# Performance work log

Measured on AMD Instinct MI355X. Metric: run time of the kernel, lower is better.

Reference implementation:

```python
import jax, jax.numpy as jnp
import numpy as np

NUM_CLASSES = 21
RMI_RADIUS = 3
POOL = 3            # rmi_pool_size == rmi_pool_stride
HALF_D = RMI_RADIUS * RMI_RADIUS
WEIGHT_LAMBDA = 0.5
CLIP_MIN = 1e-6
POS_ALPHA = 5e-4


def _max_pool(x):
    # F.max_pool2d(kernel=3, stride=3, padding=1) on NCHW
    return jax.lax.reduce_window(
        x, -jnp.inf, jax.lax.max,
        window_dimensions=(1, 1, POOL, POOL),
        window_strides=(1, 1, POOL, POOL),
        padding=[(0, 0), (0, 0), (1, 1), (1, 1)])


def _map_get_pairs(labels, probs, radius):
    # -> two tensors [N, C, radius*radius, new_h, new_w]
    h, w = labels.shape[2], labels.shape[3]
    nh, nw = h - (radius - 1), w - (radius - 1)
    la = jnp.stack([labels[:, :, y:y + nh, x:x + nw]
                    for y in range(radius) for x in range(radius)], axis=2)
    pr = jnp.stack([probs[:, :, y:y + nh, x:x + nw]
                    for y in range(radius) for x in range(radius)], axis=2)
    return la, pr


def _rmi_lower_bound(labels_4D, probs_4D):
    labels_4D = _max_pool(labels_4D)
    probs_4D = _max_pool(probs_4D)
    la, pr = _map_get_pairs(labels_4D, probs_4D, RMI_RADIUS)
    N, C = la.shape[0], la.shape[1]
    la = jax.lax.stop_gradient(la.reshape(N, C, HALF_D, -1))  # [N,C,D,M]
    pr = pr.reshape(N, C, HALF_D, -1)
    la = la - jnp.mean(la, axis=3, keepdims=True)
    pr = pr - jnp.mean(pr, axis=3, keepdims=True)
    eye = jnp.eye(HALF_D, dtype=pr.dtype) * POS_ALPHA  # broadcast over N,C
    la_cov = jnp.einsum('ncdm,ncem->ncde', la, la)
    pr_cov = jnp.einsum('ncdm,ncem->ncde', pr, pr)
    pr_cov_inv = jnp.linalg.inv(pr_cov + eye)
    la_pr_cov = jnp.einsum('ncdm,ncem->ncde', la, pr)
    appro_var = la_cov - jnp.einsum('ncde,ncef,ncgf->ncdg',
                                    la_pr_cov, pr_cov_inv, la_pr_cov)
    chol = jnp.linalg.cholesky(appro_var + eye)
    diag = jnp.diagonal(chol, axis1=-2, axis2=-1)
    rmi_now = 0.5 * 2.0 * jnp.sum(jnp.log(diag + 1e-8), axis=-1)  # [N,C]
    rmi_per_class = jnp.mean(rmi_now.reshape(-1, NUM_CLASSES), axis=0) / float(HALF_D)
    return jnp.sum(rmi_per_class)  # _IS_SUM = 1


def setup_inputs() -> dict:
    key = jax.random.key(0)
    k1, k2 = jax.random.split(key)
    logits_4D = jax.random.normal(k1, (4, NUM_CLASSES, 512, 512), dtype=jnp.float32)
    labels_4D = jax.random.randint(k2, (4, 512, 512), 0, NUM_CLASSES).astype(jnp.int64)
    return {'logits_4D': logits_4D, 'labels_4D': labels_4D}


def reference(logits_4D, labels_4D):
    # forward_sigmoid
    mask = (labels_4D < NUM_CLASSES)                       # [N,H,W] bool
    maskf = mask.astype(logits_4D.dtype)
    onehot = jax.nn.one_hot(labels_4D * mask, NUM_CLASSES,
                            dtype=logits_4D.dtype) * maskf[..., None]  # [N,H,W,C]
    onehot = jax.lax.stop_gradient(onehot)
    logits_flat = jnp.transpose(logits_4D, (0, 2, 3, 1)).reshape(-1, NUM_CLASSES)
    y_flat = onehot.reshape(-1, NUM_CLASSES)
    w_flat = maskf.reshape(-1, 1)
    valid_pixels = jnp.sum(maskf)
    # stable BCE-with-logits, sum reduction, per-pixel weight
    bce = -(y_flat * jax.nn.log_sigmoid(logits_flat)
            + (1.0 - y_flat) * jax.nn.log_sigmoid(-logits_flat))
    bce_loss = jnp.sum(bce * w_flat) / (valid_pixels + 1.0)
    probs_4D = jax.nn.sigmoid(logits_4D) * maskf[:, None, :, :] + CLIP_MIN
    labels_nchw = jnp.transpose(onehot, (0, 3, 1, 2))
    rmi_loss = _rmi_lower_bound(labels_nchw, probs_4D)
    # lambda_way == 1
    return WEIGHT_LAMBDA * bce_loss + rmi_loss * (1.0 - WEIGHT_LAMBDA)
```

## Files before the change

kernel.cpp:

```cpp
#include <hip/hip_runtime.h>
#include <math.h>
#include <stdint.h>

#define NUM_CL 21
#define NB 4
#define H 512
#define W 512
#define PH 171
#define PW 171
#define NHH 169
#define NWW 169
#define M_TOT (NHH*NWW)
#define NCP (NB*NUM_CL)
#define PPLANE (PH*PW)
#define ACC_PER 189
#define SLICES 8
#define MCHUNK ((M_TOT + SLICES - 1)/SLICES)
#define POS_ALPHA 5e-4
#define NBLKA (NB*NUM_CL*PH)

__device__ __forceinline__ int upIdx(int lo, int hi) {
    return lo*9 - (lo*(lo-1))/2 + (hi - lo);
}
__device__ __forceinline__ int tri(int d, int e) { return d*(d+1)/2 + e; }

__global__ __launch_bounds__(128) void kernelA(
    const float* __restrict__ logits, const int* __restrict__ labels,
    float* __restrict__ pooledP, unsigned char* __restrict__ pooledL,
    float* __restrict__ bce_part, unsigned int* __restrict__ cnt_part)
{
    int blk = blockIdx.x;
    int c  = blk % NUM_CL;
    int t2 = blk / NUM_CL;
    int ph = t2 % PH;
    int n  = t2 / PH;
    int q  = threadIdx.x;
    int col0 = q << 2;

    __shared__ float         svP[W];
    __shared__ unsigned char svL[W];
    __shared__ float         rbce[2];
    __shared__ unsigned int  rcnt[2];

    const float* lgp = logits + (size_t)(n*NUM_CL + c) * (H*W);
    const int*   lbp = labels + (size_t)n * (H*W);

    float vP[4] = {-INFINITY, -INFINITY, -INFINITY, -INFINITY};
    int   vL[4] = {0,0,0,0};
    float bce = 0.f;
    unsigned int cnt = 0;

    int rbase = 3*ph - 1;
    #pragma unroll
    for (int rr = 0; rr < 3; ++rr) {
        int r = rbase + rr;
        if (r < 0 || r >= H) continue;
        float4 x4 = *(const float4*)(lgp + (size_t)r*W + col0);
        int4   l4 = *(const int4*)  (lbp + (size_t)r*W + col0);
        float xs[4] = {x4.x, x4.y, x4.z, x4.w};
        int   ls[4] = {l4.x, l4.y, l4.z, l4.w};
        #pragma unroll
        for (int k = 0; k < 4; ++k) {
            int lab = ls[k];
            float x = xs[k];
            float m = (lab < NUM_CL) ? 1.f : 0.f;
            float y = (lab == c) ? 1.f : 0.f;
            float te = __expf(-fabsf(x));
            float u  = 1.f + te;
            float sp = __logf(u);
            float rc = __builtin_amdgcn_rcpf(u);
            bce += m * (fmaxf(x, 0.f) - x*y + sp);
            float sig = (x >= 0.f) ? rc : te*rc;
            float p = sig*m + 1e-6f;
            vP[k] = fmaxf(vP[k], p);
            vL[k] |= (lab == c);
            cnt += (unsigned)(lab < NUM_CL);
        }
    }

    ((float4*)svP)[q] = make_float4(vP[0], vP[1], vP[2], vP[3]);
    uchar4 u4;
    u4.x = (unsigned char)vL[0]; u4.y = (unsigned char)vL[1];
    u4.z = (unsigned char)vL[2]; u4.w = (unsigned char)vL[3];
    ((uchar4*)svL)[q] = u4;

    #pragma unroll
    for (int o = 32; o > 0; o >>= 1) {
        bce += __shfl_down(bce, o, 64);
        cnt += __shfl_down(cnt, o, 64);
    }
    int lane = threadIdx.x & 63, wv = threadIdx.x >> 6;
    if (lane == 0) { rbce[wv] = bce; rcnt[wv] = cnt; }
    __syncthreads();

    for (int pw = threadIdx.x; pw < PW; pw += 128) {
        int c0 = 3*pw - 1; if (c0 < 0) c0 = 0;
        int c1 = 3*pw + 2; if (c1 > W) c1 = W;
        float pm = -INFINITY; int lm = 0;
        for (int qq = c0; qq < c1; ++qq) {
            pm = fmaxf(pm, svP[qq]);
            lm |= svL[qq];
        }
        size_t o = ((size_t)(n*NUM_CL + c) * PH + ph) * PW + pw;
        pooledP[o] = pm;
        pooledL[o] = (unsigned char)lm;
    }

    if (threadIdx.x == 0) {
        bce_part[blk] = rbce[0] + rbce[1];
        if (c == 0) cnt_part[t2] = rcnt[0] + rcnt[1];
    }
}

__global__ __launch_bounds__(256) void kernelB(
    const float* __restrict__ pooledP, const unsigned char* __restrict__ pooledL,
    double* __restrict__ cov_acc)
{
    int nc    = blockIdx.x;
    int slice = blockIdx.y;
    int grp   = blockIdx.z;
    const float* P = pooledP + (size_t)nc * PPLANE;
    const unsigned char* L = pooledL + (size_t)nc * PPLANE;

    int mlo = slice * MCHUNK;
    int mhi = mlo + MCHUNK; if (mhi > M_TOT) mhi = M_TOT;

    __shared__ float red[4][108];
    int lane = threadIdx.x & 63;
    int wave = threadIdx.x >> 6;

    auto wred = [&](float v) -> float {
        #pragma unroll
        for (int o = 32; o > 0; o >>= 1) v += __shfl_down(v, o, 64);
        return v;
    };

    double* acc = cov_acc + (size_t)nc * ACC_PER;

    if (grp == 0) {
        float sl[9], sp[9], cll[45], cpp[45];
        #pragma unroll
        for (int d = 0; d < 9; ++d) { sl[d] = 0.f; sp[d] = 0.f; }
        #pragma unroll
        for (int k = 0; k < 45; ++k) { cll[k] = 0.f; cpp[k] = 0.f; }

        for (int m = mlo + (int)threadIdx.x; m < mhi; m += 256) {
            int i = m / NWW;
            int j = m - i * NWW;
            int base = i * PW + j;
            float la[9], pr[9];
            #pragma unroll
            for (int dy = 0; dy < 3; ++dy)
                #pragma unroll
                for (int dx = 0; dx < 3; ++dx) {
                    int o = base + dy*PW + dx;
                    pr[dy*3+dx] = P[o];
                    la[dy*3+dx] = (float)L[o];
                }
            #pragma unroll
            for (int d = 0; d < 9; ++d) { sl[d] += la[d]; sp[d] += pr[d]; }
            int k = 0;
            #pragma unroll
            for (int d = 0; d < 9; ++d)
                #pragma unroll
                for (int e = d; e < 9; ++e) {
                    cll[k] += la[d]*la[e];
                    cpp[k] += pr[d]*pr[e];
                    ++k;
                }
        }

        #pragma unroll
        for (int d = 0; d < 9; ++d) { float r = wred(sl[d]);  if (lane == 0) red[wave][d]     = r; }
        #pragma unroll
        for (int d = 0; d < 9; ++d) { float r = wred(sp[d]);  if (lane == 0) red[wave][9+d]   = r; }
        #pragma unroll
        for (int k = 0; k < 45; ++k) { float r = wred(cll[k]); if (lane == 0) red[wave][18+k] = r; }
        #pragma unroll
        for (int k = 0; k < 45; ++k) { float r = wred(cpp[k]); if (lane == 0) red[wave][63+k] = r; }
        __syncthreads();
        for (int v = threadIdx.x; v < 108; v += 256) {
            float s = red[0][v] + red[1][v] + red[2][v] + red[3][v];
            atomicAdd(&acc[v], (double)s);
        }
    } else {
        float clp[81];
        #pragma unroll
        for (int k = 0; k < 81; ++k) clp[k] = 0.f;

        for (int m = mlo + (int)threadIdx.x; m < mhi; m += 256) {
            int i = m / NWW;
            int j = m - i * NWW;
            int base = i * PW + j;
            float la[9], pr[9];
            #pragma unroll
            for (int dy = 0; dy < 3; ++dy)
                #pragma unroll
                for (int dx = 0; dx < 3; ++dx) {
                    int o = base + dy*PW + dx;
                    pr[dy*3+dx] = P[o];
                    la[dy*3+dx] = (float)L[o];
                }
            #pragma unroll
            for (int d = 0; d < 9; ++d)
                #pragma unroll
                for (int e = 0; e < 9; ++e) clp[d*9+e] += la[d]*pr[e];
        }

        #pragma unroll
        for (int k = 0; k < 81; ++k) { float r = wred(clp[k]); if (lane == 0) red[wave][k] = r; }
        __syncthreads();
        for (int v = threadIdx.x; v < 81; v += 256) {
            float s = red[0][v] + red[1][v] + red[2][v] + red[3][v];
            atomicAdd(&acc[108 + v], (double)s);
        }
    }
}

__global__ __launch_bounds__(128) void kernelC(
    const double* __restrict__ cov_acc,
    const float* __restrict__ bce_part,
    const unsigned int* __restrict__ cnt_part,
    float* __restrict__ out)
{
    int t = threadIdx.x;

    __shared__ double sb[128];
    __shared__ unsigned long long sc[128];
    double bs = 0.0;
    for (int i = t; i < NBLKA; i += 128) bs += (double)bce_part[i];
    unsigned long long cs = 0;
    for (int i = t; i < NB*PH; i += 128) cs += cnt_part[i];
    sb[t] = bs; sc[t] = cs;
    __syncthreads();
    #pragma unroll
    for (int s = 64; s > 0; s >>= 1) {
        if (t < s) { sb[t] += sb[t + s]; sc[t] += sc[t + s]; }
        __syncthreads();
    }

    float contrib = 0.f;
    if (t < NCP) {
        const double* acc = cov_acc + (size_t)t * ACC_PER;
        const double Minv = 1.0 / (double)M_TOT;
        double Sl[9], Sp[9];
        #pragma unroll
        for (int d = 0; d < 9; ++d) { Sl[d] = acc[d]; Sp[d] = acc[9+d]; }

        float A[45];
        float G[45];
        float B[81];
        #pragma unroll
        for (int d = 0; d < 9; ++d) {
            #pragma unroll
            for (int e = 0; e <= d; ++e) {
                int ku = upIdx(e, d);
                double vp = acc[63+ku] - Sp[d]*Sp[e]*Minv;
                double vl = acc[18+ku] - Sl[d]*Sl[e]*Minv;
                if (d == e) vp += POS_ALPHA;
                A[tri(d,e)] = (float)vp;
                G[tri(d,e)] = (float)vl;
            }
        }
        #pragma unroll
        for (int d = 0; d < 9; ++d) {
            #pragma unroll
            for (int e = 0; e < 9; ++e)
                B[d*9+e] = (float)(acc[108 + d*9 + e] - Sl[d]*Sp[e]*Minv);
        }

        #pragma unroll
        for (int d = 0; d < 9; ++d) {
            float s = A[tri(d,d)];
            #pragma unroll
            for (int f = 0; f < d; ++f) { float v = A[tri(d,f)]; s -= v*v; }
            float ldd = sqrtf(s);
            A[tri(d,d)] = ldd;
            float inv = 1.f / ldd;
            #pragma unroll
            for (int e = d+1; e < 9; ++e) {
                float s2 = A[tri(e,d)];
                #pragma unroll
                for (int f = 0; f < d; ++f) s2 -= A[tri(e,f)] * A[tri(d,f)];
                A[tri(e,d)] = s2 * inv;
            }
        }

        #pragma unroll
        for (int d = 0; d < 9; ++d) {
            #pragma unroll
            for (int e = 0; e < 9; ++e) {
                float s = B[d*9+e];
                #pragma unroll
                for (int f = 0; f < e; ++f) s -= A[tri(e,f)] * B[d*9+f];
                B[d*9+e] = s / A[tri(e,e)];
            }
        }

        #pragma unroll
        for (int d = 0; d < 9; ++d) {
            #pragma unroll
            for (int g = 0; g <= d; ++g) {
                float qv = 0.f;
                #pragma unroll
                for (int e = 0; e < 9; ++e) qv += B[d*9+e] * B[g*9+e];
                float v = G[tri(d,g)] - qv;
                if (d == g) v += (float)POS_ALPHA;
                G[tri(d,g)] = v;
            }
        }

        float sumlog = 0.f;
        #pragma unroll
        for (int d = 0; d < 9; ++d) {
            float s = G[tri(d,d)];
            #pragma unroll
            for (int f = 0; f < d; ++f) { float v = G[tri(d,f)]; s -= v*v; }
            float ldd = sqrtf(s);
            G[tri(d,d)] = ldd;
            sumlog += logf(ldd + 1e-8f);
            float inv = 1.f / ldd;
            #pragma unroll
            for (int e = d+1; e < 9; ++e) {
                float s2 = G[tri(e,d)];
                #pragma unroll
                for (int f = 0; f < d; ++f) s2 -= G[tri(e,f)] * G[tri(d,f)];
                G[tri(e,d)] = s2 * inv;
            }
        }
        contrib = sumlog * (1.0f / 36.0f);
    }

    __shared__ float sred[128];
    sred[t] = contrib;
    __syncthreads();
    #pragma unroll
    for (int s = 64; s > 0; s >>= 1) {
        if (t < s) sred[t] += sred[t + s];
        __syncthreads();
    }
    if (t == 0) {
        double bce_loss = sb[0] / ((double)sc[0] + 1.0);
        out[0] = (float)(0.5 * bce_loss + 0.5 * (double)sred[0]);
    }
}

extern "C" void kernel_launch(void* const* d_in, const int* in_sizes, int n_in,
                              void* d_out, int out_size, void* d_ws, size_t ws_size,
                              hipStream_t stream)
{
    (void)in_sizes; (void)n_in; (void)out_size; (void)ws_size;
    const float* logits = (const float*)d_in[0];
    const int*   labels = (const int*)d_in[1];
    float* out = (float*)d_out;

    uint8_t* w = (uint8_t*)d_ws;
    double* cov_acc = (double*)w;
    size_t off = (size_t)NCP * ACC_PER * 8;
    float* bce_part = (float*)(w + off);       off += (size_t)NBLKA * 4;
    unsigned int* cnt_part = (unsigned int*)(w + off); off += (size_t)(NB*PH) * 4;
    float* pooledP = (float*)(w + off);        off += (size_t)NCP * PPLANE * 4;
    unsigned char* pooledL = (unsigned char*)(w + off);

    hipMemsetAsync(cov_acc, 0, (size_t)NCP * ACC_PER * 8, stream);

    kernelA<<<NBLKA, 128, 0, stream>>>(logits, labels, pooledP, pooledL, bce_part, cnt_part);
    kernelB<<<dim3(NCP, SLICES, 2), 256, 0, stream>>>(pooledP, pooledL, cov_acc);
    kernelC<<<1, 128, 0, stream>>>(cov_acc, bce_part, cnt_part, out);
}
```

Baseline: 233.9 us.

## Compress labels to bytes and bitmasks, use strip-based covariance accumulation

A new pre-pass converts the int labels to a uint8 map and counts valid pixels once. Kernel A then reads 1-byte labels instead of 4-byte ones, which cuts label traffic that was re-read for each of the 21 classes. Pooled label maps are stored as 64-bit ballot bitmasks, and pooled probabilities go into rows padded to 176 for float4 loads. The covariance kernels now process 16-wide horizontal strips per thread, reusing loaded values across windows and computing the label-label statistics with popcount instead of float multiplies. The cost is an extra kernel launch and higher register pressure in the strip bodies.

```diff
diff --git a/kernel.cpp b/kernel.cpp
--- a/kernel.cpp
+++ b/kernel.cpp
@@ -8,47 +8,67 @@
 #define W 512
 #define PH 171
 #define PW 171
+#define PWPAD 176
 #define NHH 169
 #define NWW 169
 #define M_TOT (NHH*NWW)
 #define NCP (NB*NUM_CL)
-#define PPLANE (PH*PW)
 #define ACC_PER 189
-#define SLICES 8
-#define MCHUNK ((M_TOT + SLICES - 1)/SLICES)
 #define POS_ALPHA 5e-4
 #define NBLKA (NB*NUM_CL*PH)
+#define NCHUNK 11
+#define ITEMS (NHH*NCHUNK)
+#define BSLICE 8
+
+typedef unsigned long long u64;
+typedef unsigned int u32;
 
 __device__ __forceinline__ int upIdx(int lo, int hi) {
     return lo*9 - (lo*(lo-1))/2 + (hi - lo);
 }
 __device__ __forceinline__ int tri(int d, int e) { return d*(d+1)/2 + e; }
 
+__global__ __launch_bounds__(256) void kernel0(
+    const int* __restrict__ labels, unsigned char* __restrict__ lab8,
+    u64* __restrict__ validCnt)
+{
+    int idx = blockIdx.x * 256 + threadIdx.x;
+    int4 l = ((const int4*)labels)[idx];
+    uchar4 u;
+    u.x = (l.x < NUM_CL) ? (unsigned char)l.x : 255;
+    u.y = (l.y < NUM_CL) ? (unsigned char)l.y : 255;
+    u.z = (l.z < NUM_CL) ? (unsigned char)l.z : 255;
+    u.w = (l.w < NUM_CL) ? (unsigned char)l.w : 255;
+    ((uchar4*)lab8)[idx] = u;
+    u32 cnt = (l.x < NUM_CL) + (l.y < NUM_CL) + (l.z < NUM_CL) + (l.w < NUM_CL);
+    #pragma unroll
+    for (int o = 32; o > 0; o >>= 1) cnt += __shfl_down(cnt, o, 64);
+    if ((threadIdx.x & 63) == 0) atomicAdd(validCnt, (u64)cnt);
+}
+
 __global__ __launch_bounds__(128) void kernelA(
-    const float* __restrict__ logits, const int* __restrict__ labels,
-    float* __restrict__ pooledP, unsigned char* __restrict__ pooledL,
-    float* __restrict__ bce_part, unsigned int* __restrict__ cnt_part)
+    const float* __restrict__ logits, const unsigned char* __restrict__ lab8,
+    float* __restrict__ pooledP, u64* __restrict__ Lbits,
+    float* __restrict__ bce_part)
 {
     int blk = blockIdx.x;
     int c  = blk % NUM_CL;
     int t2 = blk / NUM_CL;
     int ph = t2 % PH;
     int n  = t2 / PH;
-    int q  = threadIdx.x;
-    int col0 = q << 2;
+    int tid = threadIdx.x;
+    int col0 = tid << 2;
 
     __shared__ float         svP[W];
     __shared__ unsigned char svL[W];
     __shared__ float         rbce[2];
-    __shared__ unsigned int  rcnt[2];
 
     const float* lgp = logits + (size_t)(n*NUM_CL + c) * (H*W);
-    const int*   lbp = labels + (size_t)n * (H*W);
+    const unsigned char* lbp = lab8 + (size_t)n * (H*W);
 
     float vP[4] = {-INFINITY, -INFINITY, -INFINITY, -INFINITY};
     int   vL[4] = {0,0,0,0};
     float bce = 0.f;
-    unsigned int cnt = 0;
 
     int rbase = 3*ph - 1;
     #pragma unroll
@@ -56,7 +76,7 @@
         int r = rbase + rr;
         if (r < 0 || r >= H) continue;
         float4 x4 = *(const float4*)(lgp + (size_t)r*W + col0);
-        int4   l4 = *(const int4*)  (lbp + (size_t)r*W + col0);
+        uchar4 l4 = *(const uchar4*)(lbp + (size_t)r*W + col0);
         float xs[4] = {x4.x, x4.y, x4.z, x4.w};
         int   ls[4] = {l4.x, l4.y, l4.z, l4.w};
         #pragma unroll
@@ -71,171 +91,222 @@
             float rc = __builtin_amdgcn_rcpf(u);
             bce += m * (fmaxf(x, 0.f) - x*y + sp);
             float sig = (x >= 0.f) ? rc : te*rc;
-            float p = sig*m + 1e-6f;
-            vP[k] = fmaxf(vP[k], p);
+            vP[k] = fmaxf(vP[k], sig*m + 1e-6f);
             vL[k] |= (lab == c);
-            cnt += (unsigned)(lab < NUM_CL);
-        }
-    }
-
-    ((float4*)svP)[q] = make_float4(vP[0], vP[1], vP[2], vP[3]);
+        }
+    }
+
+    ((float4*)svP)[tid] = make_float4(vP[0], vP[1], vP[2], vP[3]);
     uchar4 u4;
     u4.x = (unsigned char)vL[0]; u4.y = (unsigned char)vL[1];
     u4.z = (unsigned char)vL[2]; u4.w = (unsigned char)vL[3];
-    ((uchar4*)svL)[q] = u4;
-
-    #pragma unroll
-    for (int o = 32; o > 0; o >>= 1) {
-        bce += __shfl_down(bce, o, 64);
-        cnt += __shfl_down(cnt, o, 64);
-    }
-    int lane = threadIdx.x & 63, wv = threadIdx.x >> 6;
-    if (lane == 0) { rbce[wv] = bce; rcnt[wv] = cnt; }
+    ((uchar4*)svL)[tid] = u4;
+
+    #pragma unroll
+    for (int o = 32; o > 0; o >>= 1) bce += __shfl_down(bce, o, 64);
+    int lane = tid & 63, wv = tid >> 6;
+    if (lane == 0) rbce[wv] = bce;
     __syncthreads();
 
-    for (int pw = threadIdx.x; pw < PW; pw += 128) {
-        int c0 = 3*pw - 1; if (c0 < 0) c0 = 0;
-        int c1 = 3*pw + 2; if (c1 > W) c1 = W;
-        float pm = -INFINITY; int lm = 0;
-        for (int qq = c0; qq < c1; ++qq) {
-            pm = fmaxf(pm, svP[qq]);
-            lm |= svL[qq];
-        }
-        size_t o = ((size_t)(n*NUM_CL + c) * PH + ph) * PW + pw;
-        pooledP[o] = pm;
-        pooledL[o] = (unsigned char)lm;
-    }
-
-    if (threadIdx.x == 0) {
-        bce_part[blk] = rbce[0] + rbce[1];
-        if (c == 0) cnt_part[t2] = rcnt[0] + rcnt[1];
-    }
-}
-
-__global__ __launch_bounds__(256) void kernelB(
-    const float* __restrict__ pooledP, const unsigned char* __restrict__ pooledL,
+    size_t rowr = (size_t)(n*NUM_CL + c) * PH + ph;
+    #pragma unroll
+    for (int pass = 0; pass < 2; ++pass) {
+        int pw = tid + pass*128;
+        int lm = 0;
+        if (pw < PW) {
+            int c0 = 3*pw - 1; if (c0 < 0) c0 = 0;
+            int c1 = 3*pw + 2; if (c1 > W) c1 = W;
+            float pm = -INFINITY;
+            for (int qq = c0; qq < c1; ++qq) {
+                pm = fmaxf(pm, svP[qq]);
+                lm |= svL[qq];
+            }
+            pooledP[rowr * PWPAD + pw] = pm;
+        }
+        u64 bal = __ballot(lm != 0);
+        if (lane == 0) Lbits[rowr * 4 + (pw >> 6)] = bal;
+    }
+
+    if (tid == 0) bce_part[blk] = rbce[0] + rbce[1];
+}
+
+template<int NWIN>
+__device__ __forceinline__ void loadStrip(const float* __restrict__ P,
+                                          const u64* __restrict__ Lb,
+                                          int i, int j0,
+                                          float s[3][NWIN+2], u32 m[3])
+{
+    constexpr int NC = NWIN + 2;
+    #pragma unroll
+    for (int r = 0; r < 3; ++r) {
+        const float* rp = P + (size_t)(i + r) * PWPAD + j0;
+        #pragma unroll
+        for (int q = 0; q < NC/4; ++q) {
+            float4 v = *(const float4*)(rp + 4*q);
+            s[r][4*q+0] = v.x; s[r][4*q+1] = v.y; s[r][4*q+2] = v.z; s[r][4*q+3] = v.w;
+        }
+        #pragma unroll
+        for (int q = (NC/4)*4; q < NC; ++q) s[r][q] = rp[q];
+        const u64* lw = Lb + (size_t)(i + r) * 4 + (j0 >> 6);
+        int sh = j0 & 63;
+        u64 lo = (lw[0] >> sh) | ((lw[1] << 1) << (63 - sh));
+        m[r] = (u32)lo & 0x3FFFFu;
+    }
+}
+
+template<int NWIN>
+__device__ __forceinline__ void bodyPP(const float* __restrict__ P,
+                                       const u64* __restrict__ Lb,
+                                       int i, int j0,
+                                       float sp[9], float cpp[45],
+                                       int sl[9], int cll[45])
+{
+    float s[3][NWIN+2]; u32 m[3];
+    loadStrip<NWIN>(P, Lb, i, j0, s, m);
+    #pragma unroll
+    for (int w = 0; w < NWIN; ++w) {
+        float pv[9];
+        #pragma unroll
+        for (int d = 0; d < 9; ++d) pv[d] = s[d/3][w + d%3];
+        #pragma unroll
+        for (int d = 0; d < 9; ++d) sp[d] += pv[d];
+        int k = 0;
+        #pragma unroll
+        for (int d = 0; d < 9; ++d)
+            #pragma unroll
+            for (int e = d; e < 9; ++e) { cpp[k] += pv[d]*pv[e]; ++k; }
+    }
+    constexpr u32 WM = (1u << NWIN) - 1;
+    #pragma unroll
+    for (int d = 0; d < 9; ++d) sl[d] += __popc((m[d/3] >> (d%3)) & WM);
+    int k = 0;
+    #pragma unroll
+    for (int d = 0; d < 9; ++d) {
+        u32 md = m[d/3] >> (d%3);
+        #pragma unroll
+        for (int e = d; e < 9; ++e) { cll[k] += __popc(md & (m[e/3] >> (e%3)) & WM); ++k; }
+    }
+}
+
+template<int NWIN>
+__device__ __forceinline__ void bodyLP(const float* __restrict__ P,
+                                       const u64* __restrict__ Lb,
+                                       int i, int j0, float clp[81])
+{
+    float s[3][NWIN+2]; u32 m[3];
+    loadStrip<NWIN>(P, Lb, i, j0, s, m);
+    #pragma unroll
+    for (int w = 0; w < NWIN; ++w) {
+        float la[9], pv[9];
+        #pragma unroll
+        for (int d = 0; d < 9; ++d) {
+            pv[d] = s[d/3][w + d%3];
+            la[d] = (float)((m[d/3] >> (w + d%3)) & 1u);
+        }
+        #pragma unroll
+        for (int d = 0; d < 9; ++d)
+            #pragma unroll
+            for (int e = 0; e < 9; ++e) clp[d*9+e] += la[d]*pv[e];
+    }
+}
+
+__device__ __forceinline__ float wred64(float v) {
+    #pragma unroll
+    for (int o = 32; o > 0; o >>= 1) v += __shfl_down(v, o, 64);
+    return v;
+}
+
+__global__ __launch_bounds__(256, 2) void kernelB0(
+    const float* __restrict__ pooledP, const u64* __restrict__ Lbits,
     double* __restrict__ cov_acc)
 {
-    int nc    = blockIdx.x;
-    int slice = blockIdx.y;
-    int grp   = blockIdx.z;
-    const float* P = pooledP + (size_t)nc * PPLANE;
-    const unsigned char* L = pooledL + (size_t)nc * PPLANE;
-
-    int mlo = slice * MCHUNK;
-    int mhi = mlo + MCHUNK; if (mhi > M_TOT) mhi = M_TOT;
+    int nc = blockIdx.x;
+    int id = blockIdx.y * 256 + threadIdx.x;
+    const float* P = pooledP + (size_t)nc * PH * PWPAD;
+    const u64*  Lb = Lbits  + (size_t)nc * PH * 4;
+
+    float sp[9], cpp[45];
+    int sl[9], cll[45];
+    #pragma unroll
+    for (int d = 0; d < 9; ++d) { sp[d] = 0.f; sl[d] = 0; }
+    #pragma unroll
+    for (int k = 0; k < 45; ++k) { cpp[k] = 0.f; cll[k] = 0; }
+
+    if (id < ITEMS) {
+        int i = id / NCHUNK;
+        int chunk = id - i * NCHUNK;
+        int j0 = chunk << 4;
+        if (chunk < 10) bodyPP<16>(P, Lb, i, j0, sp, cpp, sl, cll);
+        else            bodyPP<9>(P, Lb, i, j0, sp, cpp, sl, cll);
+    }
 
     __shared__ float red[4][108];
-    int lane = threadIdx.x & 63;
-    int wave = threadIdx.x >> 6;
-
-    auto wred = [&](float v) -> float {
-        #pragma unroll
-        for (int o = 32; o > 0; o >>= 1) v += __shfl_down(v, o, 64);
-        return v;
-    };
-
+    int lane = threadIdx.x & 63, wave = threadIdx.x >> 6;
+    #pragma unroll
+    for (int d = 0; d < 9; ++d) { float r = wred64((float)sl[d]); if (lane == 0) red[wave][d]    = r; }
+    #pragma unroll
+    for (int d = 0; d < 9; ++d) { float r = wred64(sp[d]);        if (lane == 0) red[wave][9+d]  = r; }
+    #pragma unroll
+    for (int k = 0; k < 45; ++k) { float r = wred64((float)cll[k]); if (lane == 0) red[wave][18+k] = r; }
+    #pragma unroll
+    for (int k = 0; k < 45; ++k) { float r = wred64(cpp[k]);        if (lane == 0) red[wave][63+k] = r; }
+    __syncthreads();
     double* acc = cov_acc + (size_t)nc * ACC_PER;
-
-    if (grp == 0) {
-        float sl[9], sp[9], cll[45], cpp[45];
-        #pragma unroll
-        for (int d = 0; d < 9; ++d) { sl[d] = 0.f; sp[d] = 0.f; }
-        #pragma unroll
-        for (int k = 0; k < 45; ++k) { cll[k] = 0.f; cpp[k] = 0.f; }
-
-        for (int m = mlo + (int)threadIdx.x; m < mhi; m += 256) {
-            int i = m / NWW;
-            int j = m - i * NWW;
-            int base = i * PW + j;
-            float la[9], pr[9];
-            #pragma unroll
-            for (int dy = 0; dy < 3; ++dy)
-                #pragma unroll
-                for (int dx = 0; dx < 3; ++dx) {
-                    int o = base + dy*PW + dx;
-                    pr[dy*3+dx] = P[o];
-                    la[dy*3+dx] = (float)L[o];
-                }
-            #pragma unroll
-            for (int d = 0; d < 9; ++d) { sl[d] += la[d]; sp[d] += pr[d]; }
-            int k = 0;
-            #pragma unroll
-            for (int d = 0; d < 9; ++d)
-                #pragma unroll
-                for (int e = d; e < 9; ++e) {
-                    cll[k] += la[d]*la[e];
-                    cpp[k] += pr[d]*pr[e];
-                    ++k;
-                }
-        }
-
-        #pragma unroll
-        for (int d = 0; d < 9; ++d) { float r = wred(sl[d]);  if (lane == 0) red[wave][d]     = r; }
-        #pragma unroll
-        for (int d = 0; d < 9; ++d) { float r = wred(sp[d]);  if (lane == 0) red[wave][9+d]   = r; }
-        #pragma unroll
-        for (int k = 0; k < 45; ++k) { float r = wred(cll[k]); if (lane == 0) red[wave][18+k] = r; }
-        #pragma unroll
-        for (int k = 0; k < 45; ++k) { float r = wred(cpp[k]); if (lane == 0) red[wave][63+k] = r; }
-        __syncthreads();
-        for (int v = threadIdx.x; v < 108; v += 256) {
-            float s = red[0][v] + red[1][v] + red[2][v] + red[3][v];
-            atomicAdd(&acc[v], (double)s);
-        }
-    } else {
-        float clp[81];
-        #pragma unroll
-        for (int k = 0; k < 81; ++k) clp[k] = 0.f;
-
-        for (int m = mlo + (int)threadIdx.x; m < mhi; m += 256) {
-            int i = m / NWW;
-            int j = m - i * NWW;
-            int base = i * PW + j;
-            float la[9], pr[9];
-            #pragma unroll
-            for (int dy = 0; dy < 3; ++dy)
-                #pragma unroll
-                for (int dx = 0; dx < 3; ++dx) {
-                    int o = base + dy*PW + dx;
-                    pr[dy*3+dx] = P[o];
-                    la[dy*3+dx] = (float)L[o];
-                }
-            #pragma unroll
-            for (int d = 0; d < 9; ++d)
-                #pragma unroll
-                for (int e = 0; e < 9; ++e) clp[d*9+e] += la[d]*pr[e];
-        }
-
-        #pragma unroll
-        for (int k = 0; k < 81; ++k) { float r = wred(clp[k]); if (lane == 0) red[wave][k] = r; }
-        __syncthreads();
-        for (int v = threadIdx.x; v < 81; v += 256) {
-            float s = red[0][v] + red[1][v] + red[2][v] + red[3][v];
-            atomicAdd(&acc[108 + v], (double)s);
-        }
-    }
-}
-
-__global__ __launch_bounds__(128) void kernelC(
+    for (int v = threadIdx.x; v < 108; v += 256) {
+        float sum = red[0][v] + red[1][v] + red[2][v] + red[3][v];
+        atomicAdd(&acc[v], (double)sum);
+    }
+}
+
+__global__ __launch_bounds__(256, 2) void kernelB1(
+    const float* __restrict__ pooledP, const u64* __restrict__ Lbits,
+    double* __restrict__ cov_acc)
+{
+    int nc = blockIdx.x;
+    int id = blockIdx.y * 256 + threadIdx.x;
+    const float* P = pooledP + (size_t)nc * PH * PWPAD;
+    const u64*  Lb = Lbits  + (size_t)nc * PH * 4;
+
+    float clp[81];
+    #pragma unroll
+    for (int k = 0; k < 81; ++k) clp[k] = 0.f;
+
+    if (id < ITEMS) {
+        int i = id / NCHUNK;
+        int chunk = id - i * NCHUNK;
+        int j0 = chunk << 4;
+        if (chunk < 10) bodyLP<16>(P, Lb, i, j0, clp);
+        else            bodyLP<9>(P, Lb, i, j0, clp);
+    }
+
+    __shared__ float red[4][81];
+    int lane = threadIdx.x & 63, wave = threadIdx.x >> 6;
+    #pragma unroll
+    for (int k = 0; k < 81; ++k) { float r = wred64(clp[k]); if (lane == 0) red[wave][k] = r; }
+    __syncthreads();
+    double* acc = cov_acc + (size_t)nc * ACC_PER;
+    for (int v = threadIdx.x; v < 81; v += 256) {
+        float sum = red[0][v] + red[1][v] + red[2][v] + red[3][v];
+        atomicAdd(&acc[108 + v], (double)sum);
+    }
+}
+
+__global__ __launch_bounds__(256) void kernelC(
     const double* __restrict__ cov_acc,
     const float* __restrict__ bce_part,
-    const unsigned int* __restrict__ cnt_part,
+    const u64* __restrict__ validCnt,
     float* __restrict__ out)
 {
     int t = threadIdx.x;
 
-    __shared__ double sb[128];
-    __shared__ unsigned long long sc[128];
+    __shared__ double sb[256];
     double bs = 0.0;
-    for (int i = t; i < NBLKA; i += 128) bs += (double)bce_part[i];
-    unsigned long long cs = 0;
-    for (int i = t; i < NB*PH; i += 128) cs += cnt_part[i];
-    sb[t] = bs; sc[t] = cs;
+    for (int i = t; i < NBLKA; i += 256) bs += (double)bce_part[i];
+    sb[t] = bs;
     __syncthreads();
     #pragma unroll
-    for (int s = 64; s > 0; s >>= 1) {
-        if (t < s) { sb[t] += sb[t + s]; sc[t] += sc[t + s]; }
+    for (int s = 128; s > 0; s >>= 1) {
+        if (t < s) sb[t] += sb[t + s];
         __syncthreads();
     }
 
@@ -331,16 +402,16 @@
         contrib = sumlog * (1.0f / 36.0f);
     }
 
-    __shared__ float sred[128];
+    __shared__ float sred[256];
     sred[t] = contrib;
     __syncthreads();
     #pragma unroll
-    for (int s = 64; s > 0; s >>= 1) {
+    for (int s = 128; s > 0; s >>= 1) {
         if (t < s) sred[t] += sred[t + s];
         __syncthreads();
     }
     if (t == 0) {
-        double bce_loss = sb[0] / ((double)sc[0] + 1.0);
+        double bce_loss = sb[0] / ((double)validCnt[0] + 1.0);
         out[0] = (float)(0.5 * bce_loss + 0.5 * (double)sred[0]);
     }
 }
@@ -355,16 +426,20 @@
     float* out = (float*)d_out;
 
     uint8_t* w = (uint8_t*)d_ws;
-    double* cov_acc = (double*)w;
-    size_t off = (size_t)NCP * ACC_PER * 8;
+    size_t off = 0;
+    double* cov_acc = (double*)(w + off);      off += (size_t)NCP * ACC_PER * 8;
+    u64* validCnt = (u64*)(w + off);           off += 8;
     float* bce_part = (float*)(w + off);       off += (size_t)NBLKA * 4;
-    unsigned int* cnt_part = (unsigned int*)(w + off); off += (size_t)(NB*PH) * 4;
-    float* pooledP = (float*)(w + off);        off += (size_t)NCP * PPLANE * 4;
-    unsigned char* pooledL = (unsigned char*)(w + off);
-
-    hipMemsetAsync(cov_acc, 0, (size_t)NCP * ACC_PER * 8, stream);
-
-    kernelA<<<NBLKA, 128, 0, stream>>>(logits, labels, pooledP, pooledL, bce_part, cnt_part);
-    kernelB<<<dim3(NCP, SLICES, 2), 256, 0, stream>>>(pooledP, pooledL, cov_acc);
-    kernelC<<<1, 128, 0, stream>>>(cov_acc, bce_part, cnt_part, out);
-}
+    off = (off + 15) & ~(size_t)15;
+    float* pooledP = (float*)(w + off);        off += (size_t)NCP * PH * PWPAD * 4;
+    u64* Lbits = (u64*)(w + off);              off += (size_t)NCP * PH * 4 * 8;
+    unsigned char* lab8 = (unsigned char*)(w + off); off += (size_t)NB * H * W;
+
+    hipMemsetAsync(d_ws, 0, (size_t)NCP * ACC_PER * 8 + 8, stream);
+
+    kernel0<<<(NB*H*W/4 + 255)/256, 256, 0, stream>>>(labels, lab8, validCnt);
+    kernelA<<<NBLKA, 128, 0, stream>>>(logits, lab8, pooledP, Lbits, bce_part);
+    kernelB0<<<dim3(NCP, BSLICE), 256, 0, stream>>>(pooledP, Lbits, cov_acc);
+    kernelB1<<<dim3(NCP, BSLICE), 256, 0, stream>>>(pooledP, Lbits, cov_acc);
+    kernelC<<<1, 256, 0, stream>>>(cov_acc, bce_part, validCnt, out);
+}
```

New measurement: 340.2 us. 1.45x slower.
